# Performance work log

Measured on AMD Instinct MI355X. Metric: run time of the kernel, lower is better.

## Reference

```python
import jax, jax.numpy as jnp
import numpy as np

N_HEADS = 16


def setup_inputs() -> dict:
    key = jax.random.key(0)
    k1, k2, k3 = jax.random.split(key, 3)
    B, T, C = 4, 2048, 1024
    x = jax.random.normal(k1, (B, T, C), dtype=jnp.float32)
    # torch nn.Linear weights are (out_features, in_features); y = x @ W.T
    w_in = jax.random.normal(k2, (3 * C, C), dtype=jnp.float32) * 0.02
    w_out = jax.random.normal(k3, (C, C), dtype=jnp.float32) * 0.02
    return {"x": x, "w_in": w_in, "w_out": w_out}


def reference(x, w_in, w_out):
    B, T, C = x.shape
    H = N_HEADS
    hd = C // H

    qkv = x @ w_in.T                      # [B, T, 3C]
    q, k, v = jnp.split(qkv, 3, axis=2)   # each [B, T, C]

    def heads(t):
        return t.reshape(B, T, H, hd).transpose(0, 2, 1, 3)  # [B, H, T, hd]

    q, k, v = heads(q), heads(k), heads(v)

    scale = 1.0 / jnp.sqrt(jnp.float32(hd))
    scores = jnp.einsum('bhqd,bhkd->bhqk', q, k) * scale      # [B, H, T, T]
    causal = jnp.tril(jnp.ones((T, T), dtype=bool))
    scores = jnp.where(causal, scores, -jnp.inf)
    attn = jax.nn.softmax(scores, axis=-1)
    y = jnp.einsum('bhqk,bhkd->bhqd', attn, v)                # [B, H, T, hd]
    y = y.transpose(0, 2, 1, 3).reshape(B, T, C)
    return y @ w_out.T
```

## Files before the change

kernel.cpp:

```cpp
#include <hip/hip_runtime.h>
#include <stdint.h>

#define BB 4
#define TT 2048
#define CC 1024
#define HH 16
#define HD 64
#define C3 3072
#define MM (BB*TT)

typedef __bf16 bf16_t;
typedef bf16_t bf16x8 __attribute__((ext_vector_type(8)));
typedef float f32x4 __attribute__((ext_vector_type(4)));
typedef unsigned short u16;
typedef u16 u16x8 __attribute__((ext_vector_type(8)));
typedef uint32_t u32;

static __device__ __forceinline__ u16 f2bf(float f){
  u32 u = __builtin_bit_cast(u32, f);
  u32 r = (u + 0x7fffu + ((u >> 16) & 1u)) >> 16;
  return (u16)r;
}

static __device__ __forceinline__ f32x4 mfma16(bf16x8 a, bf16x8 b, f32x4 c){
  return __builtin_amdgcn_mfma_f32_16x16x32_bf16(a, b, c, 0, 0, 0);
}

typedef __attribute__((address_space(1))) void* gas_t;
typedef __attribute__((address_space(3))) void* las_t;
static __device__ __forceinline__ void gload16(const void* g, void* l){
  __builtin_amdgcn_global_load_lds((gas_t)g, (las_t)l, 16, 0, 0);
}

__global__ __launch_bounds__(256) void cvt_all(const float* __restrict__ x,
                                               const float* __restrict__ wi,
                                               const float* __restrict__ wo,
                                               u16* __restrict__ out){
  const int n1 = MM*CC/8, n2 = C3*CC/8, n3 = CC*CC/8;
  const int total = n1 + n2 + n3;
  int stride = gridDim.x * blockDim.x;
  for (int i = blockIdx.x * blockDim.x + threadIdx.x; i < total; i += stride){
    const float* src; int k;
    if (i < n1){ src = x; k = i; }
    else if (i < n1 + n2){ src = wi; k = i - n1; }
    else { src = wo; k = i - n1 - n2; }
    const float4* p = (const float4*)src + (size_t)k * 2;
    float4 a = p[0], b = p[1];
    u16x8 o;
    o[0]=f2bf(a.x); o[1]=f2bf(a.y); o[2]=f2bf(a.z); o[3]=f2bf(a.w);
    o[4]=f2bf(b.x); o[5]=f2bf(b.y); o[6]=f2bf(b.z); o[7]=f2bf(b.w);
    *((u16x8*)out + i) = o;
  }
}

template<int OUTBF>
__global__ __launch_bounds__(256) void gemm_bt(const u16* __restrict__ A,
                                               const u16* __restrict__ Bm,
                                               void* __restrict__ Cp,
                                               int M, int N, int K,
                                               int nbx, int cpx){
  __shared__ u16 As[2][128*64];
  __shared__ u16 Bs[2][128*64];
  const int bid = blockIdx.x;
  const int nb = (bid & 7) * cpx + (bid >> 3);
  const int by = nb / nbx, bx = nb - by * nbx;
  const int tid  = threadIdx.x;
  const int lane = tid & 63;
  const int w    = tid >> 6;
  const int m0   = by * 128;
  const int n0   = bx * 128;
  const int wm   = (w >> 1) * 64;
  const int wn   = (w & 1) * 64;
  const int lr   = lane & 15;
  const int lg4  = lane >> 4;

  f32x4 acc[4][4] = {};

  const int rq  = tid >> 3;
  const int c8s = ((tid & 7) ^ (rq & 7)) * 8;
  const u16* gA = A  + (size_t)(m0 + rq) * K + c8s;
  const u16* gB = Bm + (size_t)(n0 + rq) * K + c8s;

  auto stage = [&](int buf, int t){
    char* lA = (char*)&As[buf][0] + tid*16;
    char* lB = (char*)&Bs[buf][0] + tid*16;
    #pragma unroll
    for (int q = 0; q < 4; q++){
      gload16(gA + (size_t)(q*32)*K + t*64, lA + q*4096);
      gload16(gB + (size_t)(q*32)*K + t*64, lB + q*4096);
    }
  };

  stage(0, 0);

  const int NT = K >> 6;
  for (int t = 0; t < NT; t++){
    const int c = t & 1;
    asm volatile("s_waitcnt vmcnt(0)" ::: "memory");
    __builtin_amdgcn_s_barrier();
    __builtin_amdgcn_sched_barrier(0);
    if (t + 1 < NT) stage(c ^ 1, t + 1);
    #pragma unroll
    for (int kk = 0; kk < 2; kk++){
      bf16x8 af[4], bfr[4];
      #pragma unroll
      for (int m = 0; m < 4; m++){
        int row = wm + m*16 + lr;
        int slot = ((kk<<2) | lg4) ^ (row & 7);
        af[m] = *(const bf16x8*)((const char*)&As[c][0] + row*128 + slot*16);
      }
      #pragma unroll
      for (int n = 0; n < 4; n++){
        int row = wn + n*16 + lr;
        int slot = ((kk<<2) | lg4) ^ (row & 7);
        bfr[n] = *(const bf16x8*)((const char*)&Bs[c][0] + row*128 + slot*16);
      }
      __builtin_amdgcn_s_setprio(1);
      #pragma unroll
      for (int m = 0; m < 4; m++)
        #pragma unroll
        for (int n = 0; n < 4; n++)
          acc[m][n] = mfma16(af[m], bfr[n], acc[m][n]);
      __builtin_amdgcn_s_setprio(0);
    }
    __builtin_amdgcn_s_barrier();
  }

  const int cr = lg4 * 4;
  #pragma unroll
  for (int m = 0; m < 4; m++)
    #pragma unroll
    for (int n = 0; n < 4; n++)
      #pragma unroll
      for (int j = 0; j < 4; j++){
        size_t row = (size_t)(m0 + wm + m*16 + cr + j);
        size_t col = (size_t)(n0 + wn + n*16 + lr);
        if (OUTBF) ((u16*)Cp)[row*(size_t)N + col] = f2bf(acc[m][n][j]);
        else       ((float*)Cp)[row*(size_t)N + col] = acc[m][n][j];
      }
}

__global__ __launch_bounds__(256, 2) void attn_fwd(const u16* __restrict__ qkv,
                                                   u16* __restrict__ y){
  __shared__ u16 Kl[2][64*72];
  __shared__ u16 Vt[2][64*72];
  const int bid = blockIdx.x;
  const int tq = bid >> 6;
  const int h = bid & 15, b = (bid >> 4) & 3;
  const int tid = threadIdx.x, lane = tid & 63, w = tid >> 6;
  const int lr = lane & 15, lg = lane >> 4;
  const size_t base = (size_t)b * TT * C3;
  const int qA = tq*64 + w*16;
  const int qB = (31-tq)*64 + w*16;
  const float SC = 0.18033688011112042f;

  bf16x8 qf[2][2];
  {
    const u16* qp0 = qkv + base + (size_t)(qA + lr) * C3 + h*HD;
    qf[0][0] = *(const bf16x8*)(qp0 + lg*8);
    qf[0][1] = *(const bf16x8*)(qp0 + 32 + lg*8);
    const u16* qp1 = qkv + base + (size_t)(qB + lr) * C3 + h*HD;
    qf[1][0] = *(const bf16x8*)(qp1 + lg*8);
    qf[1][1] = *(const bf16x8*)(qp1 + 32 + lg*8);
    #pragma unroll
    for (int m = 0; m < 2; m++)
      #pragma unroll
      for (int i = 0; i < 2; i++)
        #pragma unroll
        for (int e = 0; e < 8; e++)
          qf[m][i][e] = (bf16_t)((float)qf[m][i][e] * SC);
  }

  const int rK = tid >> 3, cK = tid & 7;
  const int rp = tid & 15;
  const int dc = (tid >> 4) & 7;
  const int hf = tid >> 7;
  const u16* gK = qkv + base + (size_t)rK * C3 + CC + h*HD + cK*8;
  const u16* gV = qkv + base + (size_t)(2*rp + 32*hf) * C3 + 2*CC + h*HD + dc*8;

  const int kkey = ((rK >> 3) & 1) << 5;
  const int kw0 = rK*72 + ((cK*8) ^ kkey);
  const int kw1 = (rK+32)*72 + ((cK*8) ^ kkey);
  const int vcol = ((2*rp + 32*hf) ^ (8*dc)) ^ (32*(dc & 1));

  const int rdx = ((lr >> 2) & 1) << 5;
  const int rbase = 8*(lr >> 2) + (lr & 3);

  u16x8 kreg[2], vreg[2];
  kreg[0] = *(const u16x8*)(gK);
  kreg[1] = *(const u16x8*)(gK + (size_t)32*C3);
  vreg[0] = *(const u16x8*)(gV);
  vreg[1] = *(const u16x8*)(gV + C3);

  f32x4 o[2][4] = {};
  float mj[2] = {-1e30f, -1e30f};
  float lj[2] = {0.f, 0.f};

  const int ktmax = 31 - tq;
  for (int kt = 0; kt <= ktmax; kt++){
    const int cb = kt & 1;
    u16* KL = Kl[cb];
    u16* VT = Vt[cb];
    *(u16x8*)&KL[kw0] = kreg[0];
    *(u16x8*)&KL[kw1] = kreg[1];
    #pragma unroll
    for (int e = 0; e < 8; e++){
      u32 pk = (u32)vreg[0][e] | ((u32)vreg[1][e] << 16);
      *(u32*)&VT[(dc*8+e)*72 + vcol] = pk;
    }
    __syncthreads();

    if (kt < ktmax){
      const u16* gk2 = gK + (size_t)(kt+1)*64*C3;
      const u16* gv2 = gV + (size_t)(kt+1)*64*C3;
      kreg[0] = *(const u16x8*)(gk2);
      kreg[1] = *(const u16x8*)(gk2 + (size_t)32*C3);
      vreg[0] = *(const u16x8*)(gv2);
      vreg[1] = *(const u16x8*)(gv2 + C3);
    }

    const bool m0act = (kt <= tq);
    bf16x8 vb[8];

    #pragma unroll
    for (int m = 1; m >= 0; m--){
      if (m == 0 && !m0act) continue;

      f32x4 s[4] = {};
      __builtin_amdgcn_s_setprio(1);
      #pragma unroll
      for (int n = 0; n < 4; n++){
        const int rho = 32*(n>>1) + 4*(n&1) + rbase;
        bf16x8 kb0 = *(const bf16x8*)&KL[rho*72 + ((     lg*8) ^ rdx)];
        bf16x8 kb1 = *(const bf16x8*)&KL[rho*72 + ((32 + lg*8) ^ rdx)];
        s[n] = mfma16(kb0, qf[m][0], s[n]);
        s[n] = mfma16(kb1, qf[m][1], s[n]);
      }
      __builtin_amdgcn_s_setprio(0);

      if (m == 1){
        #pragma unroll
        for (int n = 0; n < 4; n++){
          const int dcr = (2*n + (lr >> 3)) & 7;
          const int c0 = ((lg ^ dcr) ^ (4 * (dcr & 1))) * 8;
          vb[2*n]   = *(const bf16x8*)&VT[(n*16+lr)*72 + c0];
          vb[2*n+1] = *(const bf16x8*)&VT[(n*16+lr)*72 + (c0 ^ 32)];
        }
      }

      const int qrow = (m ? qB : qA) + lr;
      const bool dm = (kt == (m ? ktmax : tq));
      if (dm){
        #pragma unroll
        for (int n = 0; n < 4; n++)
          #pragma unroll
          for (int j = 0; j < 4; j++)
            if (kt*64 + 32*(n>>1) + 8*lg + 4*(n&1) + j > qrow)
              s[n][j] = -1e30f;
      }
      float x0 = fmaxf(fmaxf(s[0][0], s[0][1]), fmaxf(s[0][2], s[0][3]));
      float x1 = fmaxf(fmaxf(s[1][0], s[1][1]), fmaxf(s[1][2], s[1][3]));
      float x2 = fmaxf(fmaxf(s[2][0], s[2][1]), fmaxf(s[2][2], s[2][3]));
      float x3 = fmaxf(fmaxf(s[3][0], s[3][1]), fmaxf(s[3][2], s[3][3]));
      float tm = fmaxf(fmaxf(x0, x1), fmaxf(x2, x3));
      tm = fmaxf(tm, __shfl_xor(tm, 16, 64));
      tm = fmaxf(tm, __shfl_xor(tm, 32, 64));
      float mo = mj[m];
      if (!__all(tm <= mo + 4.0f)){
        float mn = fmaxf(mo, tm);
        float al = __builtin_amdgcn_exp2f(mo - mn);
        mj[m] = mn;
        lj[m] *= al;
        float a0 = __shfl(al, lg*4+0, 16);
        float a1 = __shfl(al, lg*4+1, 16);
        float a2 = __shfl(al, lg*4+2, 16);
        float a3 = __shfl(al, lg*4+3, 16);
        #pragma unroll
        for (int n = 0; n < 4; n++){
          o[m][n][0] *= a0; o[m][n][1] *= a1;
          o[m][n][2] *= a2; o[m][n][3] *= a3;
        }
      }
      float mm = mj[m];
      float psn[4];
      bf16x8 pa, pb;
      #pragma unroll
      for (int n = 0; n < 4; n++){
        float p0 = __builtin_amdgcn_exp2f(s[n][0] - mm);
        float p1 = __builtin_amdgcn_exp2f(s[n][1] - mm);
        float p2 = __builtin_amdgcn_exp2f(s[n][2] - mm);
        float p3 = __builtin_amdgcn_exp2f(s[n][3] - mm);
        psn[n] = (p0 + p1) + (p2 + p3);
        if (n == 0){ pa[0]=(bf16_t)p0; pa[1]=(bf16_t)p1; pa[2]=(bf16_t)p2; pa[3]=(bf16_t)p3; }
        if (n == 1){ pa[4]=(bf16_t)p0; pa[5]=(bf16_t)p1; pa[6]=(bf16_t)p2; pa[7]=(bf16_t)p3; }
        if (n == 2){ pb[0]=(bf16_t)p0; pb[1]=(bf16_t)p1; pb[2]=(bf16_t)p2; pb[3]=(bf16_t)p3; }
        if (n == 3){ pb[4]=(bf16_t)p0; pb[5]=(bf16_t)p1; pb[6]=(bf16_t)p2; pb[7]=(bf16_t)p3; }
      }
      float ps = (psn[0] + psn[1]) + (psn[2] + psn[3]);
      ps += __shfl_xor(ps, 16, 64);
      ps += __shfl_xor(ps, 32, 64);
      lj[m] += ps;

      __builtin_amdgcn_s_setprio(1);
      #pragma unroll
      for (int n = 0; n < 4; n++){
        o[m][n] = mfma16(pa, vb[2*n],   o[m][n]);
        o[m][n] = mfma16(pb, vb[2*n+1], o[m][n]);
      }
      __builtin_amdgcn_s_setprio(0);
    }
  }

  #pragma unroll
  for (int m = 0; m < 2; m++){
    float inv = 1.0f / lj[m];
    float i0 = __shfl(inv, lg*4+0, 16);
    float i1 = __shfl(inv, lg*4+1, 16);
    float i2 = __shfl(inv, lg*4+2, 16);
    float i3 = __shfl(inv, lg*4+3, 16);
    const int qb = (m ? qB : qA);
    #pragma unroll
    for (int j = 0; j < 4; j++){
      float ij = (j==0) ? i0 : (j==1) ? i1 : (j==2) ? i2 : i3;
      size_t row = (size_t)b*TT + qb + lg*4 + j;
      #pragma unroll
      for (int n = 0; n < 4; n++)
        y[row*CC + h*HD + n*16 + lr] = f2bf(o[m][n][j] * ij);
    }
  }
}

extern "C" void kernel_launch(void* const* d_in, const int* in_sizes, int n_in,
                              void* d_out, int out_size, void* d_ws, size_t ws_size,
                              hipStream_t stream){
  const float* x     = (const float*)d_in[0];
  const float* w_in  = (const float*)d_in[1];
  const float* w_out = (const float*)d_in[2];
  float* out = (float*)d_out;

  u16* xb   = (u16*)d_ws;
  u16* wib  = xb  + (size_t)MM * CC;
  u16* wob  = wib + (size_t)C3 * CC;
  u16* qkvb = wob + (size_t)CC * CC;
  u16* yb   = xb;

  cvt_all<<<2048, 256, 0, stream>>>(x, w_in, w_out, xb);

  gemm_bt<1><<<1536, 256, 0, stream>>>(xb, wib, (void*)qkvb, MM, C3, CC, 24, 192);
  attn_fwd<<<1024, 256, 0, stream>>>(qkvb, yb);
  gemm_bt<0><<<512, 256, 0, stream>>>(yb, wob, (void*)out, MM, CC, CC, 8, 64);
}
```

Measured before the change: 161.9 us.

## Stage K tiles with direct global-to-LDS loads and raise attention occupancy

K tiles are now copied straight from global memory into LDS through gload16, using an XOR-swizzled unpadded layout in place of the register round-trip. This removes the K staging registers. V fragments are now re-read from LDS inside each PV step instead of being held across both query halves, which further lowers register pressure. Launch bounds are raised to 4 blocks per SM to gain occupancy. The risks are extra LDS reads for V, and any ordering problem between the asynchronous loads and the barrier.

```diff
diff --git a/kernel.cpp b/kernel.cpp
--- a/kernel.cpp
+++ b/kernel.cpp
@@ -140,9 +140,9 @@
       }
 }
 
-__global__ __launch_bounds__(256, 2) void attn_fwd(const u16* __restrict__ qkv,
+__global__ __launch_bounds__(256, 4) void attn_fwd(const u16* __restrict__ qkv,
                                                    u16* __restrict__ y){
-  __shared__ u16 Kl[2][64*72];
+  __shared__ u16 Kl[2][64*64];
   __shared__ u16 Vt[2][64*72];
   const int bid = blockIdx.x;
   const int tq = bid >> 6;
@@ -171,26 +171,27 @@
           qf[m][i][e] = (bf16_t)((float)qf[m][i][e] * SC);
   }
 
-  const int rK = tid >> 3, cK = tid & 7;
+  const int rq  = tid >> 3;
+  const int c8k = ((tid & 7) ^ (rq & 7)) * 8;
+  const u16* gK = qkv + base + (size_t)rq * C3 + CC + h*HD + c8k;
   const int rp = tid & 15;
   const int dc = (tid >> 4) & 7;
   const int hf = tid >> 7;
-  const u16* gK = qkv + base + (size_t)rK * C3 + CC + h*HD + cK*8;
   const u16* gV = qkv + base + (size_t)(2*rp + 32*hf) * C3 + 2*CC + h*HD + dc*8;
-
-  const int kkey = ((rK >> 3) & 1) << 5;
-  const int kw0 = rK*72 + ((cK*8) ^ kkey);
-  const int kw1 = (rK+32)*72 + ((cK*8) ^ kkey);
   const int vcol = ((2*rp + 32*hf) ^ (8*dc)) ^ (32*(dc & 1));
 
-  const int rdx = ((lr >> 2) & 1) << 5;
+  auto stageK = [&](int buf, int kt1){
+    const u16* g0 = gK + (size_t)(kt1*64) * C3;
+    gload16(g0,                  (char*)&Kl[buf][0] + tid*16);
+    gload16(g0 + (size_t)32*C3,  (char*)&Kl[buf][0] + 4096 + tid*16);
+  };
+
   const int rbase = 8*(lr >> 2) + (lr & 3);
 
-  u16x8 kreg[2], vreg[2];
-  kreg[0] = *(const u16x8*)(gK);
-  kreg[1] = *(const u16x8*)(gK + (size_t)32*C3);
+  u16x8 vreg[2];
   vreg[0] = *(const u16x8*)(gV);
   vreg[1] = *(const u16x8*)(gV + C3);
+  stageK(0, 0);
 
   f32x4 o[2][4] = {};
   float mj[2] = {-1e30f, -1e30f};
@@ -199,10 +200,8 @@
   const int ktmax = 31 - tq;
   for (int kt = 0; kt <= ktmax; kt++){
     const int cb = kt & 1;
-    u16* KL = Kl[cb];
+    const u16* KL = Kl[cb];
     u16* VT = Vt[cb];
-    *(u16x8*)&KL[kw0] = kreg[0];
-    *(u16x8*)&KL[kw1] = kreg[1];
     #pragma unroll
     for (int e = 0; e < 8; e++){
       u32 pk = (u32)vreg[0][e] | ((u32)vreg[1][e] << 16);
@@ -211,16 +210,13 @@
     __syncthreads();
 
     if (kt < ktmax){
-      const u16* gk2 = gK + (size_t)(kt+1)*64*C3;
+      stageK(cb ^ 1, kt + 1);
       const u16* gv2 = gV + (size_t)(kt+1)*64*C3;
-      kreg[0] = *(const u16x8*)(gk2);
-      kreg[1] = *(const u16x8*)(gk2 + (size_t)32*C3);
       vreg[0] = *(const u16x8*)(gv2);
       vreg[1] = *(const u16x8*)(gv2 + C3);
     }
 
     const bool m0act = (kt <= tq);
-    bf16x8 vb[8];
 
     #pragma unroll
     for (int m = 1; m >= 0; m--){
@@ -231,22 +227,13 @@
       #pragma unroll
       for (int n = 0; n < 4; n++){
         const int rho = 32*(n>>1) + 4*(n&1) + rbase;
-        bf16x8 kb0 = *(const bf16x8*)&KL[rho*72 + ((     lg*8) ^ rdx)];
-        bf16x8 kb1 = *(const bf16x8*)&KL[rho*72 + ((32 + lg*8) ^ rdx)];
+        const int rk = rho & 7;
+        bf16x8 kb0 = *(const bf16x8*)((const char*)KL + rho*128 + ((lg     ^ rk)*16));
+        bf16x8 kb1 = *(const bf16x8*)((const char*)KL + rho*128 + (((4+lg) ^ rk)*16));
         s[n] = mfma16(kb0, qf[m][0], s[n]);
         s[n] = mfma16(kb1, qf[m][1], s[n]);
       }
       __builtin_amdgcn_s_setprio(0);
-
-      if (m == 1){
-        #pragma unroll
-        for (int n = 0; n < 4; n++){
-          const int dcr = (2*n + (lr >> 3)) & 7;
-          const int c0 = ((lg ^ dcr) ^ (4 * (dcr & 1))) * 8;
-          vb[2*n]   = *(const bf16x8*)&VT[(n*16+lr)*72 + c0];
-          vb[2*n+1] = *(const bf16x8*)&VT[(n*16+lr)*72 + (c0 ^ 32)];
-        }
-      }
 
       const int qrow = (m ? qB : qA) + lr;
       const bool dm = (kt == (m ? ktmax : tq));
@@ -304,8 +291,12 @@
       __builtin_amdgcn_s_setprio(1);
       #pragma unroll
       for (int n = 0; n < 4; n++){
-        o[m][n] = mfma16(pa, vb[2*n],   o[m][n]);
-        o[m][n] = mfma16(pb, vb[2*n+1], o[m][n]);
+        const int dcr = (2*n + (lr >> 3)) & 7;
+        const int c0 = ((lg ^ dcr) ^ (4 * (dcr & 1))) * 8;
+        bf16x8 vb0 = *(const bf16x8*)&VT[(n*16+lr)*72 + c0];
+        bf16x8 vb1 = *(const bf16x8*)&VT[(n*16+lr)*72 + (c0 ^ 32)];
+        o[m][n] = mfma16(pa, vb0, o[m][n]);
+        o[m][n] = mfma16(pb, vb1, o[m][n]);
       }
       __builtin_amdgcn_s_setprio(0);
     }
```

After: 160.9 us (median of 2 runs). Within noise of the previous version (-0.6%).
